# Kernel optimization log

Hardware: AMD Instinct MI355X
Metric: run time of the kernel (lower is better)

The kernel has to match this reference:

```python
import jax, jax.numpy as jnp
import numpy as np
import math

N0, E, D_IN, H, NC, UH = 4096, 65536, 128, 256, 10, 64
K1 = math.ceil(0.8 * N0)   # 3277 nodes kept by pool1
K2 = math.ceil(0.2 * K1)   # 656 nodes kept by pool2

PARAM_SHAPES = dict(
    gcn1_w=(D_IN, H), gcn1_b=(H,), pool1_w=(H,), gcn2_w=(H, H), gcn2_b=(H,), pool2_w=(H,),
    inr_w=(H, H), inr_b=(H,), ini_w=(H, H), ini_b=(H,),
    enc1_w=(1, UH), enc1_b=(UH,), enc2_w=(UH, UH), enc2_b=(UH,),
    p1_w=(UH, UH), p1_b=(UH,), p2_w=(UH, UH // 2), p2_b=(UH // 2,),
    p3_w=(UH // 2, K2 * K2), p3_b=(K2 * K2,),
    rt_w=(H, H), rt_b=(H,), it_w=(H, H), it_b=(H,),
    msg_wr=(H, H), msg_wi=(H, H),
    mc1_w=(H, H // 2), mc1_b=(H // 2,), mc2_w=(H // 2, NC), mc2_b=(NC,),
    pc1_w=(H, H // 2), pc1_b=(H // 2,), pc2_w=(H // 2, NC), pc2_b=(NC,),
)

def gcn_conv(x, src, dst, emask, W, b):
    # GCNConv: self-loops + symmetric normalization; emask zeroes edges dropped by pooling
    n = x.shape[0]
    h = x @ W
    deg = jnp.zeros((n,), h.dtype).at[dst].add(emask) + 1.0
    dis = jax.lax.rsqrt(deg)
    coef = dis[src] * dis[dst] * emask
    out = jnp.zeros_like(h).at[dst].add(coef[:, None] * h[src])
    out = out + (dis * dis)[:, None] * h   # self-loop contribution
    return out + b

def topk_pool(x, src, dst, emask, w, k):
    # PyG TopKPooling: score = x@w/||w||, keep top-k, x <- x[perm]*tanh(score[perm])
    n = x.shape[0]
    score = (x @ w) / jnp.linalg.norm(w)
    _, perm = jax.lax.top_k(score, k)
    x_new = x[perm] * jnp.tanh(score[perm])[:, None]
    mapping = jnp.full((n,), -1, jnp.int32).at[perm].set(jnp.arange(k, dtype=jnp.int32))
    ns, nd = mapping[src], mapping[dst]
    nm = emask * (ns >= 0) * (nd >= 0)
    return x_new, jnp.maximum(ns, 0), jnp.maximum(nd, 0), nm

def herm_sqrt(C):
    C = (C + C.conj().T) * 0.5
    w, V = jnp.linalg.eigh(C)
    w = jnp.maximum(w, 0.0)
    return (V * jnp.sqrt(w + 1e-8)) @ V.conj().T

def forward(x, edge_index, P):
    src, dst = edge_index[0], edge_index[1]
    em = jnp.ones((src.shape[0],), jnp.float32)
    h = jax.nn.relu(gcn_conv(x, src, dst, em, P['gcn1_w'], P['gcn1_b']))
    h, src, dst, em = topk_pool(h, src, dst, em, P['pool1_w'], K1)
    h = jax.nn.relu(gcn_conv(h, src, dst, em, P['gcn2_w'], P['gcn2_b']))
    h, src, dst, em = topk_pool(h, src, dst, em, P['pool2_w'], K2)
    xr = h @ P['inr_w'] + P['inr_b']
    xi = h @ P['ini_w'] + P['ini_b']
    # --- LocalQuantumLayer (eval mode: dropout is identity) ---
    # ImprovedUnitaryDilationNetwork on the pooled graph (N = K2)
    xg = jnp.ones((K2, 1), jnp.float32)
    xg = jax.nn.relu(gcn_conv(xg, src, dst, em, P['enc1_w'], P['enc1_b']))
    xg = gcn_conv(xg, src, dst, em, P['enc2_w'], P['enc2_b'])
    emb = xg.mean(0)                                     # global_mean_pool, single graph
    t = jax.nn.relu(emb @ P['p1_w'] + P['p1_b'])
    t = jax.nn.relu(t @ P['p2_w'] + P['p2_b'])
    pm = jnp.tanh(t @ P['p3_w'] + P['p3_b']).reshape(K2, K2)
    A = 0.05 * ((pm - pm.T) * 0.5 + 1j * (pm + pm.T) * 0.5)  # antihermitian, scaled
    U = jax.scipy.linalg.expm(A)
    I = jnp.eye(K2, dtype=U.dtype)
    S1 = jax.lax.stop_gradient(herm_sqrt(I - U.conj().T @ U))
    S2 = jax.lax.stop_gradient(herm_sqrt(I - U @ U.conj().T))
    U_dil = jnp.concatenate([jnp.concatenate([U, S1], 1),
                             jnp.concatenate([S2, -U.conj().T], 1)], 0)
    xrt = jax.nn.relu(xr @ P['rt_w'] + P['rt_b'])
    xit = jax.nn.relu(xi @ P['it_w'] + P['it_b'])
    xc = xrt + 1j * xit
    # unitary_dim = 2*K2 > K2 nodes -> single batch, U_sub = U_dil[:K2,:K2]
    evolved = U_dil[:K2, :K2] @ xc
    Wm = P['msg_wr'] + 1j * P['msg_wi']
    msg = evolved[src] @ Wm                              # message(x_j) = x_j @ W (complex)
    agg = jnp.zeros_like(xc).at[dst].add(msg * em[:, None])  # aggr='add'
    outc = agg + (xr + 1j * xi)                          # identity residual (dims equal)
    mag = jnp.abs(outc)
    ph = jnp.arctan2(outc.imag, outc.real)
    gm, gp = mag.mean(0), ph.mean(0)                     # global_mean_pool, single graph
    lm = jax.nn.relu(gm @ P['mc1_w'] + P['mc1_b']) @ P['mc2_w'] + P['mc2_b']
    lp = jax.nn.relu(gp @ P['pc1_w'] + P['pc1_b']) @ P['pc2_w'] + P['pc2_b']
    return lm + lp

def setup_inputs() -> dict:
    key = jax.random.key(0)
    ks = iter(jax.random.split(key, 64))
    inp = {}
    inp['x'] = jax.random.normal(next(ks), (N0, D_IN), jnp.float32)
    inp['edge_index'] = jax.random.randint(next(ks), (2, E), 0, N0)
    for name, shp in PARAM_SHAPES.items():
        inp[name] = jax.random.normal(next(ks), shp, jnp.float32) * 0.05
    return inp

def reference(x, edge_index, gcn1_w, gcn1_b, pool1_w, gcn2_w, gcn2_b, pool2_w, inr_w, inr_b, ini_w, ini_b, enc1_w, enc1_b, enc2_w, enc2_b, p1_w, p1_b, p2_w, p2_b, p3_w, p3_b, rt_w, rt_b, it_w, it_b, msg_wr, msg_wi, mc1_w, mc1_b, mc2_w, mc2_b, pc1_w, pc1_b, pc2_w, pc2_b):
    P = dict(locals())
    x_ = P.pop('x'); ei = P.pop('edge_index')
    return forward(x_, ei, P)
```

## Files before the change

### kernel.cpp

```cpp
#include <hip/hip_runtime.h>
#include <cstddef>
#include <utility>

constexpr int N0  = 4096;
constexpr int E   = 65536;
constexpr int DIN = 128;
constexpr int HD  = 256;
constexpr int NC  = 10;
constexpr int UHD = 64;
constexpr int K1  = 3277;
constexpr int K2  = 656;
constexpr int PMN = K2 * K2;

constexpr int SQ_SLOTS = 4;

constexpr int PLD = 704;
constexpr size_t PPS = (size_t)PLD * PLD;

constexpr int CSPLIT = 8;

#define F4(n) ((size_t)(n) * 4)
constexpr size_t O_H1    = 0;
constexpr size_t O_OUT1  = O_H1    + F4(N0 * HD);
constexpr size_t O_DEG1  = O_OUT1  + F4(N0 * HD);
constexpr size_t O_DIS1  = O_DEG1  + F4(N0);
constexpr size_t O_SC1   = O_DIS1  + F4(N0);
constexpr size_t O_PERM1 = O_SC1   + F4(N0);
constexpr size_t O_MAP1  = O_PERM1 + F4(N0);
constexpr size_t O_H1P   = O_MAP1  + F4(N0);
constexpr size_t O_SRC2  = O_H1P   + F4(K1 * HD);
constexpr size_t O_DST2  = O_SRC2  + F4(E);
constexpr size_t O_EM2   = O_DST2  + F4(E);
constexpr size_t O_H2    = O_EM2   + F4(E);
constexpr size_t O_OUT2  = O_H2    + F4(K1 * HD);
constexpr size_t O_DEG2  = O_OUT2  + F4(K1 * HD);
constexpr size_t O_DIS2  = O_DEG2  + F4(N0);
constexpr size_t O_SC2   = O_DIS2  + F4(N0);
constexpr size_t O_PERM2 = O_SC2   + F4(N0);
constexpr size_t O_MAP2  = O_PERM2 + F4(N0);
constexpr size_t O_H2P   = O_MAP2  + F4(N0);
constexpr size_t O_SRC3  = O_H2P   + F4(K2 * HD);
constexpr size_t O_DST3  = O_SRC3  + F4(E);
constexpr size_t O_EM3   = O_DST3  + F4(E);
constexpr size_t O_XR    = O_EM3   + F4(E);
constexpr size_t O_XI    = O_XR    + F4(K2 * HD);
constexpr size_t O_DEG3  = O_XI    + F4(K2 * HD);
constexpr size_t O_DIS3  = O_DEG3  + F4(1024);
constexpr size_t O_SCOEF = O_DIS3  + F4(1024);
constexpr size_t O_XG1   = O_SCOEF + F4(1024);
constexpr size_t O_XG2H  = O_XG1   + F4(K2 * UHD);
constexpr size_t O_XG2   = O_XG2H  + F4(K2 * UHD);
constexpr size_t O_EMB   = O_XG2   + F4(K2 * UHD);
constexpr size_t O_T1    = O_EMB   + F4(64);
constexpr size_t O_T2    = O_T1    + F4(64);
constexpr size_t O_NORM  = O_T2    + F4(64);
constexpr size_t O_PM    = O_NORM  + F4(64);
constexpr size_t O_BM    = O_PM    + F4(PMN);
constexpr size_t O_P0    = O_BM    + F4(PMN) * 2;
constexpr size_t O_P1    = O_P0    + F4(PMN) * 2;
constexpr size_t O_XRT   = O_P1    + F4(PMN) * 2;
constexpr size_t O_XIT   = O_XRT   + F4(K2 * HD);
constexpr size_t O_XC    = O_XIT   + F4(K2 * HD);
constexpr size_t O_EVO   = O_XC    + F4(K2 * HD) * 2;
constexpr size_t O_AGG0  = O_EVO   + F4(K2 * HD) * 2;
constexpr size_t O_WC    = O_AGG0  + F4(K2 * HD) * 2;
constexpr size_t O_AGG1  = O_WC    + F4(HD * HD) * 2;
constexpr size_t O_MAG   = O_AGG1  + F4(K2 * HD) * 2;
constexpr size_t O_PH    = O_MAG   + F4(K2 * HD);
constexpr size_t O_GM    = O_PH    + F4(K2 * HD);
constexpr size_t O_GP    = O_GM    + F4(256);
constexpr size_t O_HM    = O_GP    + F4(256);
constexpr size_t O_HP    = O_HM    + F4(256);
constexpr size_t O_LM    = O_HP    + F4(256);
constexpr size_t O_LP    = O_LM    + F4(64);
constexpr size_t WS_NEED = O_LP    + F4(64);

constexpr size_t O_SA = 0;
constexpr size_t O_ST = O_SA + PPS * 2 * 4;
static_assert(O_ST + PPS * 2 * 4 <= O_SRC3, "SA/ST must fit in dead region");

constexpr size_t O_B2 = O_XRT;
static_assert(O_B2 + F4(PMN) * 2 <= O_MAG, "B2 must fit in XRT..AGG1 region");

constexpr size_t O_CSR_OFF = O_MAG;
constexpr size_t O_CSR_CUR = O_CSR_OFF + F4(4104);
constexpr size_t O_CSR_SRC = O_CSR_CUR + F4(4104);
constexpr size_t O_CSR_CF  = O_CSR_SRC + F4(E);
static_assert(O_CSR_CF + F4(E) <= O_GM, "CSR must fit in MAG/PH region");

constexpr size_t O_PARTX  = (WS_NEED + 255) & ~(size_t)255;
constexpr size_t PART_SZ  = (size_t)CSPLIT * PMN * 8;
constexpr size_t WS_TOTAL = O_PARTX + PART_SZ;

typedef __attribute__((ext_vector_type(8))) short s8v;
typedef __attribute__((ext_vector_type(4))) float f4v;

__device__ inline unsigned short f2bf(float x) {
  unsigned u = __float_as_uint(x);
  u += 0x7FFFu + ((u >> 16) & 1u);
  return (unsigned short)(u >> 16);
}
__device__ inline float bf2f(unsigned short h) {
  return __uint_as_float(((unsigned)h) << 16);
}
__device__ inline void split4(float re, float im, unsigned short* out,
                              size_t ps, size_t o) {
  unsigned short rh = f2bf(re);
  unsigned short rl = f2bf(re - bf2f(rh));
  unsigned short ih = f2bf(im);
  unsigned short il = f2bf(im - bf2f(ih));
  out[o] = rh; out[ps + o] = rl; out[2 * ps + o] = ih; out[3 * ps + o] = il;
}


template <int ACT>
__global__ void rmm64(const float* __restrict__ A, const float* __restrict__ B,
                      const float* __restrict__ bias, float* __restrict__ C,
                      int M, int N, int K, int CS, int CO) {
  __shared__ float As[64][17];
  __shared__ float Bs[16][64];
  int t  = threadIdx.x;
  int tx = t & 15, ty = t >> 4;
  int bm = blockIdx.y * 64, bn = blockIdx.x * 64;
  float acc[4][4] = {};
  for (int kt = 0; kt < K; kt += 16) {
#pragma unroll
    for (int i = 0; i < 4; i++) {
      int l = t + i * 256;
      int kk = l & 15, mm = l >> 4;
      int gr = bm + mm;
      As[mm][kk] = (gr < M) ? A[(size_t)gr * K + kt + kk] : 0.f;
    }
#pragma unroll
    for (int i = 0; i < 4; i++) {
      int l = t + i * 256;
      int cc = l & 63, kk = l >> 6;
      int gc = bn + cc;
      Bs[kk][cc] = (gc < N) ? B[(size_t)(kt + kk) * N + gc] : 0.f;
    }
    __syncthreads();
#pragma unroll
    for (int kk = 0; kk < 16; kk++) {
      float a[4], b[4];
#pragma unroll
      for (int i = 0; i < 4; i++) a[i] = As[ty + 16 * i][kk];
#pragma unroll
      for (int j = 0; j < 4; j++) b[j] = Bs[kk][tx + 16 * j];
#pragma unroll
      for (int i = 0; i < 4; i++)
#pragma unroll
        for (int j = 0; j < 4; j++) acc[i][j] += a[i] * b[j];
    }
    __syncthreads();
  }
#pragma unroll
  for (int i = 0; i < 4; i++) {
    int r = bm + ty + 16 * i;
    if (r >= M) continue;
#pragma unroll
    for (int j = 0; j < 4; j++) {
      int c = bn + tx + 16 * j;
      if (c >= N) continue;
      float v = acc[i][j] + (bias ? bias[c] : 0.f);
      if (ACT == 1) v = fmaxf(v, 0.f);
      C[((size_t)r * N + c) * CS + CO] = v;
    }
  }
}

template <int ACT>
__global__ void rmm64_dual(const float* __restrict__ A0, const float* __restrict__ A1,
                           const float* __restrict__ B0, const float* __restrict__ B1,
                           const float* __restrict__ b0, const float* __restrict__ b1,
                           float* __restrict__ C0, float* __restrict__ C1,
                           int M, int N, int K, int CS) {
  const float* A = blockIdx.z ? A1 : A0;
  const float* B = blockIdx.z ? B1 : B0;
  const float* bias = blockIdx.z ? b1 : b0;
  float* C = blockIdx.z ? C1 : C0;
  __shared__ float As[64][17];
  __shared__ float Bs[16][64];
  int t  = threadIdx.x;
  int tx = t & 15, ty = t >> 4;
  int bm = blockIdx.y * 64, bn = blockIdx.x * 64;
  float acc[4][4] = {};
  for (int kt = 0; kt < K; kt += 16) {
#pragma unroll
    for (int i = 0; i < 4; i++) {
      int l = t + i * 256;
      int kk = l & 15, mm = l >> 4;
      int gr = bm + mm;
      As[mm][kk] = (gr < M) ? A[(size_t)gr * K + kt + kk] : 0.f;
    }
#pragma unroll
    for (int i = 0; i < 4; i++) {
      int l = t + i * 256;
      int cc = l & 63, kk = l >> 6;
      int gc = bn + cc;
      Bs[kk][cc] = (gc < N) ? B[(size_t)(kt + kk) * N + gc] : 0.f;
    }
    __syncthreads();
#pragma unroll
    for (int kk = 0; kk < 16; kk++) {
      float a[4], b[4];
#pragma unroll
      for (int i = 0; i < 4; i++) a[i] = As[ty + 16 * i][kk];
#pragma unroll
      for (int j = 0; j < 4; j++) b[j] = Bs[kk][tx + 16 * j];
#pragma unroll
      for (int i = 0; i < 4; i++)
#pragma unroll
        for (int j = 0; j < 4; j++) acc[i][j] += a[i] * b[j];
    }
    __syncthreads();
  }
#pragma unroll
  for (int i = 0; i < 4; i++) {
    int r = bm + ty + 16 * i;
    if (r >= M) continue;
#pragma unroll
    for (int j = 0; j < 4; j++) {
      int c = bn + tx + 16 * j;
      if (c >= N) continue;
      float v = acc[i][j] + (bias ? bias[c] : 0.f);
      if (ACT == 1) v = fmaxf(v, 0.f);
      C[((size_t)r * N + c) * CS] = v;
    }
  }
}

__global__ void split_planesT(const float2* __restrict__ in, int inM, int inN,
                              unsigned short* __restrict__ out, int padR, int ld,
                              size_t ps) {
  __shared__ float2 tile[32][33];
  int tx = threadIdx.x & 31, ty = threadIdx.x >> 5;
  int k0 = blockIdx.x * 32, n0 = blockIdx.y * 32;
  for (int i = ty; i < 32; i += 8) {
    int k = k0 + i, n = n0 + tx;
    tile[i][tx] = (k < inM && n < inN) ? in[(size_t)k * inN + n]
                                       : make_float2(0.f, 0.f);
  }
  __syncthreads();
  for (int i = ty; i < 32; i += 8) {
    int n = n0 + i, k = k0 + tx;
    if (n < padR && k < ld)
      split4(tile[tx][i].x, tile[tx][i].y, out, ps, (size_t)n * ld + k);
  }
}

__global__ void split_planesT2(const float* __restrict__ re, const float* __restrict__ im,
                               int inM, int inN, unsigned short* __restrict__ out,
                               int padR, int ld, size_t ps) {
  __shared__ float2 tile[32][33];
  int tx = threadIdx.x & 31, ty = threadIdx.x >> 5;
  int k0 = blockIdx.x * 32, n0 = blockIdx.y * 32;
  for (int i = ty; i < 32; i += 8) {
    int k = k0 + i, n = n0 + tx;
    tile[i][tx] = (k < inM && n < inN)
        ? make_float2(re[(size_t)k * inN + n], im[(size_t)k * inN + n])
        : make_float2(0.f, 0.f);
  }
  __syncthreads();
  for (int i = ty; i < 32; i += 8) {
    int n = n0 + i, k = k0 + tx;
    if (n < padR && k < ld)
      split4(tile[tx][i].x, tile[tx][i].y, out, ps, (size_t)n * ld + k);
  }
}

__global__ __launch_bounds__(256, 2) void cmm_bf16_sk(
    const unsigned short* __restrict__ SA, size_t psA, int ldA,
    const unsigned short* __restrict__ ST, size_t psT, int ldT,
    float2* __restrict__ Part, int M, int N, int Kp, int chunk,
    const int* __restrict__ gate, int slot) {
  if (gate && slot >= *gate - 1) return;
  int k0 = blockIdx.x * chunk;
  int kend = min(Kp, k0 + chunk);
  int t = threadIdx.x;
  int wave = t >> 6, lane = t & 63;
  int quad = lane >> 4, mn = lane & 15;
  int rowA = blockIdx.z * 64 + wave * 16 + mn;
  int bn = blockIdx.y * 64;
  const unsigned short* a0 = SA + (size_t)rowA * ldA;
  f4v accR[4], accI[4];
#pragma unroll
  for (int i = 0; i < 4; i++) {
    accR[i] = (f4v){0.f, 0.f, 0.f, 0.f};
    accI[i] = (f4v){0.f, 0.f, 0.f, 0.f};
  }
  s8v cA[4], cB[4][4], nA[4], nB[4][4];
  {
    int ka = k0 + quad * 8;
#pragma unroll
    for (int p = 0; p < 4; p++) cA[p] = *(const s8v*)(a0 + p * psA + ka);
#pragma unroll
    for (int tl = 0; tl < 4; tl++) {
      const unsigned short* b0 = ST + (size_t)(bn + tl * 16 + mn) * ldT + ka;
#pragma unroll
      for (int p = 0; p < 4; p++) cB[tl][p] = *(const s8v*)(b0 + p * psT);
    }
  }
  for (int kt = k0; kt < kend; kt += 32) {
    int kn = kt + 32;
    if (kn < kend) {
      int ka = kn + quad * 8;
#pragma unroll
      for (int p = 0; p < 4; p++) nA[p] = *(const s8v*)(a0 + p * psA + ka);
#pragma unroll
      for (int tl = 0; tl < 4; tl++) {
        const unsigned short* b0 = ST + (size_t)(bn + tl * 16 + mn) * ldT + ka;
#pragma unroll
        for (int p = 0; p < 4; p++) nB[tl][p] = *(const s8v*)(b0 + p * psT);
      }
    }
    s8v nih, nil_;
#pragma unroll
    for (int q = 0; q < 8; q++) {
      nih[q]  = (short)(cA[2][q] ^ (short)0x8000);
      nil_[q] = (short)(cA[3][q] ^ (short)0x8000);
    }
#pragma unroll
    for (int tl = 0; tl < 4; tl++) {
      f4v r = accR[tl];
      r = __builtin_amdgcn_mfma_f32_16x16x32_bf16(cA[0], cB[tl][0], r, 0, 0, 0);
      r = __builtin_amdgcn_mfma_f32_16x16x32_bf16(cA[1], cB[tl][0], r, 0, 0, 0);
      r = __builtin_amdgcn_mfma_f32_16x16x32_bf16(cA[0], cB[tl][1], r, 0, 0, 0);
      r = __builtin_amdgcn_mfma_f32_16x16x32_bf16(nih, cB[tl][2], r, 0, 0, 0);
      r = __builtin_amdgcn_mfma_f32_16x16x32_bf16(nil_, cB[tl][2], r, 0, 0, 0);
      r = __builtin_amdgcn_mfma_f32_16x16x32_bf16(nih, cB[tl][3], r, 0, 0, 0);
      accR[tl] = r;
      f4v im = accI[tl];
      im = __builtin_amdgcn_mfma_f32_16x16x32_bf16(cA[0], cB[tl][2], im, 0, 0, 0);
      im = __builtin_amdgcn_mfma_f32_16x16x32_bf16(cA[1], cB[tl][2], im, 0, 0, 0);
      im = __builtin_amdgcn_mfma_f32_16x16x32_bf16(cA[0], cB[tl][3], im, 0, 0, 0);
      im = __builtin_amdgcn_mfma_f32_16x16x32_bf16(cA[2], cB[tl][0], im, 0, 0, 0);
      im = __builtin_amdgcn_mfma_f32_16x16x32_bf16(cA[3], cB[tl][0], im, 0, 0, 0);
      im = __builtin_amdgcn_mfma_f32_16x16x32_bf16(cA[2], cB[tl][1], im, 0, 0, 0);
      accI[tl] = im;
    }
    if (kn < kend) {
#pragma unroll
      for (int p = 0; p < 4; p++) cA[p] = nA[p];
#pragma unroll
      for (int tl = 0; tl < 4; tl++)
#pragma unroll
        for (int p = 0; p < 4; p++) cB[tl][p] = nB[tl][p];
    }
  }
  float2* P = Part + (size_t)blockIdx.x * M * N;
#pragma unroll
  for (int tl = 0; tl < 4; tl++) {
    int col = bn + tl * 16 + mn;
    if (col >= N) continue;
#pragma unroll
    for (int r = 0; r < 4; r++) {
      int row = blockIdx.z * 64 + wave * 16 + quad * 4 + r;
      if (row >= M) continue;
      P[(size_t)row * N + col] = make_float2(accR[tl][r], accI[tl][r]);
    }
  }
}

__global__ void creduce(const float2* __restrict__ Part, float2* __restrict__ C,
                        int MN, int N, int S, float e0,
                        const float2* __restrict__ E1, float e1,
                        const float2* __restrict__ E2, float e2) {
  int idx = blockIdx.x * 256 + threadIdx.x;
  if (idx >= MN) return;
  float sr = 0.f, si = 0.f;
  for (int z = 0; z < S; z++) {
    float2 p = Part[(size_t)z * MN + idx];
    sr += p.x;
    si += p.y;
  }
  if (e0 != 0.f) {
    int r = idx / N;
    if (idx - r * N == r) sr += e0;
  }
  if (E1) { float2 b = E1[idx]; sr += e1 * b.x; si += e1 * b.y; }
  if (E2) { float2 b = E2[idx]; sr += e2 * b.x; si += e2 * b.y; }
  C[idx] = make_float2(sr, si);
}

template <int WC_, int WSA, int WST>
__global__ void creduce_tiled(const float2* __restrict__ Part, int S, int M, int N,
                              int RP, int CP, float2* __restrict__ C,
                              unsigned short* __restrict__ SAp, size_t psA,
                              unsigned short* __restrict__ STp, size_t psT,
                              float e0, const float2* __restrict__ E1, float e1,
                              const float2* __restrict__ E2, float e2,
                              const int* __restrict__ gate, int slot) {
  if (gate && slot >= *gate - 1) return;
  __shared__ float vr[32][33], vi[32][33];
  int tx = threadIdx.x & 31, ty = threadIdx.x >> 5;
  int r0 = blockIdx.y * 32, c0 = blockIdx.x * 32;
  size_t MN = (size_t)M * N;
  for (int i = ty; i < 32; i += 8) {
    int r = r0 + i, c = c0 + tx;
    float sr = 0.f, si = 0.f;
    if (r < M && c < N) {
      size_t o = (size_t)r * N + c;
      for (int z = 0; z < S; z++) {
        float2 p = Part[z * MN + o];
        sr += p.x;
        si += p.y;
      }
      if (e0 != 0.f && r == c) sr += e0;
      if (E1) { float2 b = E1[o]; sr += e1 * b.x; si += e1 * b.y; }
      if (E2) { float2 b = E2[o]; sr += e2 * b.x; si += e2 * b.y; }
      if (WC_) C[o] = make_float2(sr, si);
    }
    if (WSA) split4(sr, si, SAp, psA, (size_t)r * CP + c);
    if (WST) { vr[i][tx] = sr; vi[i][tx] = si; }
  }
  if (WST) {
    __syncthreads();
    for (int i = ty; i < 32; i += 8) {
      int c = c0 + i, r = r0 + tx;
      split4(vr[tx][i], vi[tx][i], STp, psT, (size_t)c * RP + r);
    }
  }
}

__global__ void build_B_split(const float* __restrict__ pm, int n,
                              const float* __restrict__ scale_p,
                              float2* __restrict__ BM,
                              unsigned short* __restrict__ SAp,
                              unsigned short* __restrict__ STp, size_t ps,
                              int RP, int CP) {
  __shared__ float vr[32][33], vi[32][33];
  float scale = scale_p[0];
  int tx = threadIdx.x & 31, ty = threadIdx.x >> 5;
  int r0 = blockIdx.y * 32, c0 = blockIdx.x * 32;
  for (int i = ty; i < 32; i += 8) {
    int r = r0 + i, c = c0 + tx;
    float sr = 0.f, si = 0.f;
    if (r < n && c < n) {
      float pij = pm[(size_t)r * n + c];
      float pji = pm[(size_t)c * n + r];
      sr = scale * (pij - pji);
      si = scale * (pij + pji);
      BM[(size_t)r * n + c] = make_float2(sr, si);
    }
    split4(sr, si, SAp, ps, (size_t)r * CP + c);
    vr[i][tx] = sr;
    vi[i][tx] = si;
  }
  __syncthreads();
  for (int i = ty; i < 32; i += 8) {
    int c = c0 + i, r = r0 + tx;
    split4(vr[tx][i], vi[tx][i], STp, ps, (size_t)c * RP + r);
  }
}

__global__ void anorm_rows(const float* __restrict__ pm, int n,
                           int* __restrict__ anrm) {
  int i = blockIdx.x;
  __shared__ float red[256];
  float s = 0.f;
  for (int j = threadIdx.x; j < n; j += 256) {
    float pij = pm[(size_t)i * n + j];
    float pji = pm[(size_t)j * n + i];
    float a = pij - pji, b = pij + pji;
    s += sqrtf(a * a + b * b);
  }
  red[threadIdx.x] = s;
  __syncthreads();
  for (int off = 128; off > 0; off >>= 1) {
    if (threadIdx.x < off) red[threadIdx.x] += red[threadIdx.x + off];
    __syncthreads();
  }
  if (threadIdx.x == 0) atomicMax(anrm, __float_as_int(red[0] * 0.025f));
}

__global__ void finalize_s(const int* __restrict__ anrm, int* __restrict__ sdev,
                           float* __restrict__ scale) {
  float a = __int_as_float(*anrm);
  int s = (int)ceilf(log2f(fmaxf(a, 1e-20f) / 1.4f));
  s = min(max(s, 1), SQ_SLOTS + 1);
  *sdev = s;
  *scale = 0.025f * exp2f(-(float)s);
}

__global__ void combo3_planes(const float2* __restrict__ Bp, const float2* __restrict__ B2p,
                              unsigned short* __restrict__ planes, size_t ps,
                              int M, int N, int padR, int ld,
                              float e0, float e1, float e2) {
  int idx = blockIdx.x * 256 + threadIdx.x;
  if (idx >= padR * ld) return;
  int r = idx / ld, c = idx - r * ld;
  float sr = 0.f, si = 0.f;
  if (r < M && c < N) {
    size_t o = (size_t)r * N + c;
    float2 b = Bp[o], b2 = B2p[o];
    sr = e1 * b.x + e2 * b2.x;
    si = e1 * b.y + e2 * b2.y;
    if (r == c) sr += e0;
  }
  split4(sr, si, planes, ps, idx);
}

__global__ void hist_edges(const int* __restrict__ dst, const float* __restrict__ em,
                           int* __restrict__ cnt) {
  int e = blockIdx.x * 256 + threadIdx.x;
  if (e >= E) return;
  float m = em ? em[e] : 1.0f;
  if (m != 0.f) atomicAdd(&cnt[dst[e]], 1);
}

__global__ __launch_bounds__(1024) void scan_offsets(const int* __restrict__ cnt, int n,
                                                     int* __restrict__ off,
                                                     int* __restrict__ cur,
                                                     float* __restrict__ dis) {
  __shared__ int sums[1024];
  int t = threadIdx.x;
  int base = t * 4;
  int v[4];
  int s = 0;
#pragma unroll
  for (int j = 0; j < 4; j++) {
    int i = base + j;
    int ci = (i < n) ? cnt[i] : 0;
    if (i < n) dis[i] = 1.0f / sqrtf((float)ci + 1.0f);
    v[j] = s;
    s += ci;
  }
  sums[t] = s;
  __syncthreads();
  for (int d = 1; d < 1024; d <<= 1) {
    int x = (t >= d) ? sums[t - d] : 0;
    __syncthreads();
    sums[t] += x;
    __syncthreads();
  }
  int pre = (t > 0) ? sums[t - 1] : 0;
#pragma unroll
  for (int j = 0; j < 4; j++) {
    int i = base + j;
    if (i < n) { int o = pre + v[j]; off[i] = o; cur[i] = o; }
  }
  if (t == 1023) off[n] = sums[1023];
}

__global__ void fill_edges(const int* __restrict__ src, const int* __restrict__ dst,
                           const float* __restrict__ em, const float* __restrict__ dis,
                           int* __restrict__ cur, int* __restrict__ esrc,
                           float* __restrict__ ecoef) {
  int e = blockIdx.x * 256 + threadIdx.x;
  if (e >= E) return;
  float m = em ? em[e] : 1.0f;
  if (m == 0.f) return;
  int s = src[e], d = dst[e];
  int pos = atomicAdd(&cur[d], 1);
  esrc[pos] = s;
  ecoef[pos] = dis[s] * dis[d];
}

template <int ACT>
__global__ void gcn_gather(const int* __restrict__ off, const int* __restrict__ esrc,
                           const float* __restrict__ ecoef, const float* __restrict__ Hm,
                           const float* __restrict__ dis, const float* __restrict__ bias,
                           float* __restrict__ out, int F) {
  int i = blockIdx.x;
  int e0 = off[i], e1 = off[i + 1];
  float d2 = dis[i] * dis[i];
  for (int f = threadIdx.x; f < F; f += blockDim.x) {
    float acc = d2 * Hm[(size_t)i * F + f] + bias[f];
    for (int e = e0; e < e1; e++)
      acc += ecoef[e] * Hm[(size_t)esrc[e] * F + f];
    if (ACT == 1) acc = fmaxf(acc, 0.f);
    out[(size_t)i * F + f] = acc;
  }
}

__global__ void enc1_fused(const int* __restrict__ off, const float* __restrict__ ecoef,
                           const float* __restrict__ dis, const float* __restrict__ w,
                           const float* __restrict__ b, float* __restrict__ xg1) {
  int i = blockIdx.x;
  int lane = threadIdx.x;
  float s = 0.f;
  for (int e = off[i] + lane; e < off[i + 1]; e += 64) s += ecoef[e];
#pragma unroll
  for (int d = 32; d > 0; d >>= 1) s += __shfl_xor(s, d, 64);
  float sc = s + dis[i] * dis[i];
  xg1[(size_t)i * UHD + lane] = fmaxf(sc * w[lane] + b[lane], 0.f);
}

__global__ void agg_gather_split(const int* __restrict__ off, const int* __restrict__ esrc,
                                 const float2* __restrict__ evo,
                                 unsigned short* __restrict__ planes, size_t ps,
                                 int F, int M) {
  int i = blockIdx.x;
  if (i >= M) {
    for (int f = threadIdx.x; f < F; f += blockDim.x)
      split4(0.f, 0.f, planes, ps, (size_t)i * F + f);
    return;
  }
  int e0 = off[i], e1 = off[i + 1];
  for (int f = threadIdx.x; f < F; f += blockDim.x) {
    float sr = 0.f, si = 0.f;
    for (int e = e0; e < e1; e++) {
      float2 v = evo[(size_t)esrc[e] * F + f];
      sr += v.x;
      si += v.y;
    }
    split4(sr, si, planes, ps, (size_t)i * F + f);
  }
}

__global__ void rowdot_wn(const float* __restrict__ X, const float* __restrict__ w,
                          float* __restrict__ out, int F, int n,
                          float* __restrict__ normout) {
  int i = blockIdx.x;
  __shared__ float red[256];
  float s = 0.f;
  if (i == n) {
    for (int k = threadIdx.x; k < F; k += 256) s += w[k] * w[k];
  } else {
    for (int f = threadIdx.x; f < F; f += 256) s += X[(size_t)i * F + f] * w[f];
  }
  red[threadIdx.x] = s;
  __syncthreads();
  for (int off = 128; off > 0; off >>= 1) {
    if (threadIdx.x < off) red[threadIdx.x] += red[threadIdx.x + off];
    __syncthreads();
  }
  if (threadIdx.x == 0) {
    if (i == n) normout[0] = sqrtf(red[0]);
    else out[i] = red[0];
  }
}

__global__ __launch_bounds__(1024) void bitonic_topk(const float* __restrict__ score,
                                                     int n, int* __restrict__ perm, int k,
                                                     int* __restrict__ map,
                                                     int* __restrict__ cntz, int ncnt) {
  __shared__ unsigned long long keys[4096];
  int t = threadIdx.x;
  for (int i = t; i < 4096; i += 1024) {
    unsigned long long kk = 0ull;
    if (i < n) {
      float f = score[i];
      unsigned u = __float_as_uint(f);
      u = (f >= 0.0f) ? (u | 0x80000000u) : ~u;
      kk = ((unsigned long long)u << 32) | (unsigned)(~(unsigned)i);
    }
    keys[i] = kk;
  }
  __syncthreads();
  for (int size = 2; size <= 4096; size <<= 1) {
    for (int stride = size >> 1; stride > 0; stride >>= 1) {
      for (int i = t; i < 2048; i += 1024) {
        int pos = ((i & ~(stride - 1)) << 1) | (i & (stride - 1));
        int partner = pos + stride;
        bool desc = (pos & size) == 0;
        unsigned long long a = keys[pos], b = keys[partner];
        if ((a < b) == desc) { keys[pos] = b; keys[partner] = a; }
      }
      __syncthreads();
    }
  }
  for (int i = t; i < 4096; i += 1024) {
    int idx = (int)(~(unsigned)(keys[i] & 0xFFFFFFFFull));
    if (idx >= 0) map[idx] = (i < k) ? i : -1;
    if (i < k) perm[i] = idx;
  }
  for (int i = t; i < ncnt; i += 1024) cntz[i] = 0;
}

__global__ void pool_gather(const float* __restrict__ X, const int* __restrict__ perm,
                            const float* __restrict__ dot, const float* __restrict__ normbuf,
                            float* __restrict__ Xn, int F) {
  int i = blockIdx.x;
  int p = perm[i];
  float sc = tanhf(dot[p] / normbuf[0]);
  for (int f = threadIdx.x; f < F; f += blockDim.x)
    Xn[(size_t)i * F + f] = X[(size_t)p * F + f] * sc;
}

__global__ void remap_hist(const int* __restrict__ srcIn, const int* __restrict__ dstIn,
                           const float* __restrict__ emIn, const int* __restrict__ map,
                           int* __restrict__ srcOut, int* __restrict__ dstOut,
                           float* __restrict__ emOut, int* __restrict__ cnt) {
  int e = blockIdx.x * 256 + threadIdx.x;
  if (e >= E) return;
  int ns = map[srcIn[e]], nd = map[dstIn[e]];
  float m = emIn ? emIn[e] : 1.0f;
  if (ns < 0 || nd < 0) m = 0.f;
  srcOut[e] = ns < 0 ? 0 : ns;
  dstOut[e] = nd < 0 ? 0 : nd;
  emOut[e] = m;
  if (m != 0.f) atomicAdd(&cnt[nd], 1);
}

__global__ void col_mean(const float* __restrict__ X, float* __restrict__ out,
                         int rows, int cols) {
  int c = blockIdx.x;
  __shared__ float red[256];
  float s = 0.f;
  for (int r = threadIdx.x; r < rows; r += 256) s += X[(size_t)r * cols + c];
  red[threadIdx.x] = s;
  __syncthreads();
  for (int off = 128; off > 0; off >>= 1) {
    if (threadIdx.x < off) red[threadIdx.x] += red[threadIdx.x + off];
    __syncthreads();
  }
  if (threadIdx.x == 0) out[c] = red[0] / (float)rows;
}

__global__ void magph_mean(const float2* __restrict__ agg, const float* __restrict__ xr,
                           const float* __restrict__ xi, float* __restrict__ gm,
                           float* __restrict__ gp, int rows, int cols) {
  int c = blockIdx.x;
  __shared__ float rm[256], rp[256];
  float sm = 0.f, sp = 0.f;
  for (int r = threadIdx.x; r < rows; r += 256) {
    size_t o = (size_t)r * cols + c;
    float2 a = agg[o];
    float re = a.x + xr[o];
    float im = a.y + xi[o];
    sm += sqrtf(re * re + im * im);
    sp += atan2f(im, re);
  }
  rm[threadIdx.x] = sm;
  rp[threadIdx.x] = sp;
  __syncthreads();
  for (int off = 128; off > 0; off >>= 1) {
    if (threadIdx.x < off) {
      rm[threadIdx.x] += rm[threadIdx.x + off];
      rp[threadIdx.x] += rp[threadIdx.x + off];
    }
    __syncthreads();
  }
  if (threadIdx.x == 0) {
    gm[c] = rm[0] / (float)rows;
    gp[c] = rp[0] / (float)rows;
  }
}

template <int ACT>
__global__ void vecmat(const float* __restrict__ v, const float* __restrict__ W,
                       const float* __restrict__ b, float* __restrict__ out,
                       int Kdim, int Ndim) {
  __shared__ float vs[256];
  for (int k = threadIdx.x; k < Kdim; k += blockDim.x) vs[k] = v[k];
  __syncthreads();
  for (int j = threadIdx.x; j < Ndim; j += blockDim.x) {
    float acc = b ? b[j] : 0.f;
    for (int k = 0; k < Kdim; k++) acc += vs[k] * W[(size_t)k * Ndim + j];
    out[j] = (ACT == 1) ? fmaxf(acc, 0.f) : acc;
  }
}

__global__ void vecmat_tanh_wide(const float* __restrict__ v, const float* __restrict__ W,
                                 const float* __restrict__ b, float* __restrict__ out,
                                 int Kdim, int Ndim, int* __restrict__ anrm_init) {
  __shared__ float vs[64];
  if (threadIdx.x < Kdim) vs[threadIdx.x] = v[threadIdx.x];
  if (blockIdx.x == 0 && threadIdx.x == 0) *anrm_init = 0;
  __syncthreads();
  int j = blockIdx.x * 256 + threadIdx.x;
  if (j >= Ndim) return;
  float acc = b[j];
  for (int k = 0; k < Kdim; k++) acc += vs[k] * W[(size_t)k * Ndim + j];
  out[j] = tanhf(acc);
}

__global__ __launch_bounds__(256) void heads_fused(
    const float* __restrict__ GM, const float* __restrict__ GP,
    const float* __restrict__ mc1_w, const float* __restrict__ mc1_b,
    const float* __restrict__ mc2_w, const float* __restrict__ mc2_b,
    const float* __restrict__ pc1_w, const float* __restrict__ pc1_b,
    const float* __restrict__ pc2_w, const float* __restrict__ pc2_b,
    float* __restrict__ out) {
  __shared__ float g[256], h[128], acc[NC];
  int t = threadIdx.x;
  if (t < NC) acc[t] = 0.f;
  for (int pass = 0; pass < 2; pass++) {
    const float* gv = pass ? GP : GM;
    const float* w1 = pass ? pc1_w : mc1_w;
    const float* b1 = pass ? pc1_b : mc1_b;
    const float* w2 = pass ? pc2_w : mc2_w;
    const float* b2 = pass ? pc2_b : mc2_b;
    g[t] = gv[t];
    __syncthreads();
    if (t < 128) {
      float s = b1[t];
      for (int k = 0; k < 256; k++) s += g[k] * w1[(size_t)k * 128 + t];
      h[t] = fmaxf(s, 0.f);
    }
    __syncthreads();
    if (t < NC) {
      float s = b2[t];
      for (int k = 0; k < 128; k++) s += h[k] * w2[(size_t)k * NC + t];
      acc[t] += s;
    }
    __syncthreads();
  }
  if (t < NC) out[t] = acc[t];
}

static inline int sk_chunk32(int K, int S) { return (((K + S - 1) / S) + 31) & ~31; }

extern "C" void kernel_launch(void* const* d_in, const int* in_sizes, int n_in,
                              void* d_out, int out_size, void* d_ws, size_t ws_size,
                              hipStream_t stream) {
  if (ws_size < WS_TOTAL) return;

  const float* x       = (const float*)d_in[0];
  const int*   ei      = (const int*)d_in[1];
  const float* gcn1_w  = (const float*)d_in[2];
  const float* gcn1_b  = (const float*)d_in[3];
  const float* pool1_w = (const float*)d_in[4];
  const float* gcn2_w  = (const float*)d_in[5];
  const float* gcn2_b  = (const float*)d_in[6];
  const float* pool2_w = (const float*)d_in[7];
  const float* inr_w   = (const float*)d_in[8];
  const float* inr_b   = (const float*)d_in[9];
  const float* ini_w   = (const float*)d_in[10];
  const float* ini_b   = (const float*)d_in[11];
  const float* enc1_w  = (const float*)d_in[12];
  const float* enc1_b  = (const float*)d_in[13];
  const float* enc2_w  = (const float*)d_in[14];
  const float* enc2_b  = (const float*)d_in[15];
  const float* p1_w    = (const float*)d_in[16];
  const float* p1_b    = (const float*)d_in[17];
  const float* p2_w    = (const float*)d_in[18];
  const float* p2_b    = (const float*)d_in[19];
  const float* p3_w    = (const float*)d_in[20];
  const float* p3_b    = (const float*)d_in[21];
  const float* rt_w    = (const float*)d_in[22];
  const float* rt_b    = (const float*)d_in[23];
  const float* it_w    = (const float*)d_in[24];
  const float* it_b    = (const float*)d_in[25];
  const float* msg_wr  = (const float*)d_in[26];
  const float* msg_wi  = (const float*)d_in[27];
  const float* mc1_w   = (const float*)d_in[28];
  const float* mc1_b   = (const float*)d_in[29];
  const float* mc2_w   = (const float*)d_in[30];
  const float* mc2_b   = (const float*)d_in[31];
  const float* pc1_w   = (const float*)d_in[32];
  const float* pc1_b   = (const float*)d_in[33];
  const float* pc2_w   = (const float*)d_in[34];
  const float* pc2_b   = (const float*)d_in[35];

  char* ws = (char*)d_ws;
  float*  H1    = (float*)(ws + O_H1);
  float*  OUT1  = (float*)(ws + O_OUT1);
  int*    CNT1  = (int*)(ws + O_DEG1);
  float*  DIS1  = (float*)(ws + O_DIS1);
  float*  SC1   = (float*)(ws + O_SC1);
  int*    PERM1 = (int*)(ws + O_PERM1);
  int*    MAP1  = (int*)(ws + O_MAP1);
  float*  H1P   = (float*)(ws + O_H1P);
  int*    SRC2  = (int*)(ws + O_SRC2);
  int*    DST2  = (int*)(ws + O_DST2);
  float*  EM2   = (float*)(ws + O_EM2);
  float*  H2    = (float*)(ws + O_H2);
  float*  OUT2  = (float*)(ws + O_OUT2);
  int*    CNT2  = (int*)(ws + O_DEG2);
  float*  DIS2  = (float*)(ws + O_DIS2);
  float*  SC2   = (float*)(ws + O_SC2);
  int*    PERM2 = (int*)(ws + O_PERM2);
  int*    MAP2  = (int*)(ws + O_MAP2);
  float*  H2P   = (float*)(ws + O_H2P);
  int*    SRC3  = (int*)(ws + O_SRC3);
  int*    DST3  = (int*)(ws + O_DST3);
  float*  EM3   = (float*)(ws + O_EM3);
  float*  XRb   = (float*)(ws + O_XR);
  float*  XIb   = (float*)(ws + O_XI);
  int*    CNT3  = (int*)(ws + O_DEG3);
  float*  DIS3  = (float*)(ws + O_DIS3);
  float*  XG1   = (float*)(ws + O_XG1);
  float*  XG2H  = (float*)(ws + O_XG2H);
  float*  XG2   = (float*)(ws + O_XG2);
  float*  EMB   = (float*)(ws + O_EMB);
  float*  T1    = (float*)(ws + O_T1);
  float*  T2    = (float*)(ws + O_T2);
  float*  NORM  = (float*)(ws + O_NORM);
  int*    ANRM  = (int*)(NORM + 2);
  int*    SDEV  = (int*)(NORM + 3);
  float*  SCALE = NORM + 4;
  float*  PMV   = (float*)(ws + O_PM);
  float2* BM    = (float2*)(ws + O_BM);
  float2* XC    = (float2*)(ws + O_XC);
  float2* EVO   = (float2*)(ws + O_EVO);
  float2* AGG1  = (float2*)(ws + O_AGG1);
  float*  GM    = (float*)(ws + O_GM);
  float*  GP    = (float*)(ws + O_GP);
  unsigned short* SA = (unsigned short*)(ws + O_SA);
  unsigned short* ST = (unsigned short*)(ws + O_ST);
  float2* PART  = (float2*)(ws + O_PARTX);
  float2* B2v   = (float2*)(ws + O_B2);
  int*    COFF  = (int*)(ws + O_CSR_OFF);
  int*    CCUR  = (int*)(ws + O_CSR_CUR);
  int*    CSRC  = (int*)(ws + O_CSR_SRC);
  float*  CCOEF = (float*)(ws + O_CSR_CF);

  const int* SRC1 = ei;
  const int* DST1 = ei + E;
  const int eg = E / 256;

  rmm64<0><<<dim3(HD / 64, N0 / 64), 256, 0, stream>>>(x, gcn1_w, nullptr, H1, N0, HD, DIN, 1, 0);
  hipMemsetAsync(CNT1, 0, F4(N0), stream);
  hist_edges<<<eg, 256, 0, stream>>>(DST1, nullptr, CNT1);
  scan_offsets<<<1, 1024, 0, stream>>>(CNT1, N0, COFF, CCUR, DIS1);
  fill_edges<<<eg, 256, 0, stream>>>(SRC1, DST1, nullptr, DIS1, CCUR, CSRC, CCOEF);
  gcn_gather<1><<<N0, 256, 0, stream>>>(COFF, CSRC, CCOEF, H1, DIS1, gcn1_b, OUT1, HD);

  rowdot_wn<<<N0 + 1, 256, 0, stream>>>(OUT1, pool1_w, SC1, HD, N0, NORM);
  bitonic_topk<<<1, 1024, 0, stream>>>(SC1, N0, PERM1, K1, MAP1, CNT2, K1);
  pool_gather<<<K1, 256, 0, stream>>>(OUT1, PERM1, SC1, NORM, H1P, HD);
  remap_hist<<<eg, 256, 0, stream>>>(SRC1, DST1, nullptr, MAP1, SRC2, DST2, EM2, CNT2);

  rmm64<0><<<dim3(HD / 64, (K1 + 63) / 64), 256, 0, stream>>>(H1P, gcn2_w, nullptr, H2, K1, HD, HD, 1, 0);
  scan_offsets<<<1, 1024, 0, stream>>>(CNT2, K1, COFF, CCUR, DIS2);
  fill_edges<<<eg, 256, 0, stream>>>(SRC2, DST2, EM2, DIS2, CCUR, CSRC, CCOEF);
  gcn_gather<1><<<K1, 256, 0, stream>>>(COFF, CSRC, CCOEF, H2, DIS2, gcn2_b, OUT2, HD);

  rowdot_wn<<<K1 + 1, 256, 0, stream>>>(OUT2, pool2_w, SC2, HD, K1, NORM + 1);
  bitonic_topk<<<1, 1024, 0, stream>>>(SC2, K1, PERM2, K2, MAP2, CNT3, K2);
  pool_gather<<<K2, 256, 0, stream>>>(OUT2, PERM2, SC2, NORM + 1, H2P, HD);
  remap_hist<<<eg, 256, 0, stream>>>(SRC2, DST2, EM2, MAP2, SRC3, DST3, EM3, CNT3);

  rmm64_dual<0><<<dim3(HD / 64, (K2 + 63) / 64, 2), 256, 0, stream>>>(
      H2P, H2P, inr_w, ini_w, inr_b, ini_b, XRb, XIb, K2, HD, HD, 1);

  scan_offsets<<<1, 1024, 0, stream>>>(CNT3, K2, COFF, CCUR, DIS3);
  fill_edges<<<eg, 256, 0, stream>>>(SRC3, DST3, EM3, DIS3, CCUR, CSRC, CCOEF);

  enc1_fused<<<K2, 64, 0, stream>>>(COFF, CCOEF, DIS3, enc1_w, enc1_b, XG1);
  rmm64<0><<<dim3(UHD / 64, (K2 + 63) / 64), 256, 0, stream>>>(XG1, enc2_w, nullptr, XG2H, K2, UHD, UHD, 1, 0);
  gcn_gather<0><<<K2, 64, 0, stream>>>(COFF, CSRC, CCOEF, XG2H, DIS3, enc2_b, XG2, UHD);
  col_mean<<<UHD, 256, 0, stream>>>(XG2, EMB, K2, UHD);

  vecmat<1><<<1, 256, 0, stream>>>(EMB, p1_w, p1_b, T1, UHD, UHD);
  vecmat<1><<<1, 256, 0, stream>>>(T1, p2_w, p2_b, T2, UHD, UHD / 2);
  vecmat_tanh_wide<<<(PMN + 255) / 256, 256, 0, stream>>>(T2, p3_w, p3_b, PMV, UHD / 2, PMN, ANRM);
  anorm_rows<<<K2, 256, 0, stream>>>(PMV, K2, ANRM);
  finalize_s<<<1, 1, 0, stream>>>(ANRM, SDEV, SCALE);

  const int sgrid = (PLD * PLD + 255) / 256;
  const dim3 tg22(PLD / 32, PLD / 32);
  const int chF = sk_chunk32(PLD, CSPLIT);
  const dim3 gBig(CSPLIT, 11, 11);
  const float c3 = 1.f / 6.f, c4 = 1.f / 24.f, c5 = 1.f / 120.f;
  const float c6 = 1.f / 720.f, c7 = 1.f / 5040.f, c8 = 1.f / 40320.f;
  const float c9 = 1.f / 362880.f, c10 = 1.f / 3628800.f, c11 = 1.f / 39916800.f;

  build_B_split<<<tg22, 256, 0, stream>>>(PMV, K2, SCALE, BM, SA, ST, PPS, PLD, PLD);
  cmm_bf16_sk<<<gBig, 256, 0, stream>>>(SA, PPS, PLD, ST, PPS, PLD, PART, K2, K2, PLD, chF, nullptr, 0);
  creduce_tiled<1, 1, 0><<<tg22, 256, 0, stream>>>(PART, CSPLIT, K2, K2, PLD, PLD,
      B2v, SA, PPS, nullptr, 0, 0.f, nullptr, 0.f, nullptr, 0.f, nullptr, 0);
  cmm_bf16_sk<<<gBig, 256, 0, stream>>>(SA, PPS, PLD, ST, PPS, PLD, PART, K2, K2, PLD, chF, nullptr, 0);
  creduce_tiled<0, 0, 1><<<tg22, 256, 0, stream>>>(PART, CSPLIT, K2, K2, PLD, PLD,
      nullptr, nullptr, 0, ST, PPS, 0.f, nullptr, 0.f, nullptr, 0.f, nullptr, 0);
  combo3_planes<<<sgrid, 256, 0, stream>>>(BM, B2v, SA, PPS, K2, K2, PLD, PLD, c9, c10, c11);
  cmm_bf16_sk<<<gBig, 256, 0, stream>>>(SA, PPS, PLD, ST, PPS, PLD, PART, K2, K2, PLD, chF, nullptr, 0);
  creduce_tiled<0, 1, 0><<<tg22, 256, 0, stream>>>(PART, CSPLIT, K2, K2, PLD, PLD,
      nullptr, SA, PPS, nullptr, 0, c6, BM, c7, B2v, c8, nullptr, 0);
  cmm_bf16_sk<<<gBig, 256, 0, stream>>>(SA, PPS, PLD, ST, PPS, PLD, PART, K2, K2, PLD, chF, nullptr, 0);
  creduce_tiled<0, 1, 0><<<tg22, 256, 0, stream>>>(PART, CSPLIT, K2, K2, PLD, PLD,
      nullptr, SA, PPS, nullptr, 0, c3, BM, c4, B2v, c5, nullptr, 0);
  cmm_bf16_sk<<<gBig, 256, 0, stream>>>(SA, PPS, PLD, ST, PPS, PLD, PART, K2, K2, PLD, chF, nullptr, 0);
  creduce_tiled<0, 1, 1><<<tg22, 256, 0, stream>>>(PART, CSPLIT, K2, K2, PLD, PLD,
      nullptr, SA, PPS, ST, PPS, 1.f, BM, 1.f, B2v, 0.5f, nullptr, 0);
  for (int t = 0; t < SQ_SLOTS; ++t) {
    cmm_bf16_sk<<<gBig, 256, 0, stream>>>(SA, PPS, PLD, ST, PPS, PLD, PART, K2, K2, PLD, chF, SDEV, t);
    creduce_tiled<0, 1, 1><<<tg22, 256, 0, stream>>>(PART, CSPLIT, K2, K2, PLD, PLD,
        nullptr, SA, PPS, ST, PPS, 0.f, nullptr, 0.f, nullptr, 0.f, SDEV, t);
  }

  rmm64_dual<1><<<dim3(HD / 64, (K2 + 63) / 64, 2), 256, 0, stream>>>(
      XRb, XIb, rt_w, it_w, rt_b, it_b, (float*)XC, (float*)XC + 1, K2, HD, HD, 2);
  {
    const int mn = K2 * HD;
    const int rg = (mn + 255) / 256;
    const dim3 gSkin(CSPLIT, HD / 64, 11);
    const size_t psX = (size_t)HD * PLD;
    split_planesT<<<dim3((PLD + 31) / 32, (HD + 31) / 32), 256, 0, stream>>>(
        XC, K2, HD, ST, HD, PLD, psX);
    cmm_bf16_sk<<<gSkin, 256, 0, stream>>>(SA, PPS, PLD, ST, psX, PLD, PART, K2, HD, PLD, chF, nullptr, 0);
    creduce_tiled<0, 0, 1><<<dim3(HD / 32, PLD / 32), 256, 0, stream>>>(
        PART, CSPLIT, K2, HD, PLD, HD, nullptr, nullptr, 0, ST, psX,
        0.f, nullptr, 0.f, nullptr, 0.f, nullptr, 0);
    cmm_bf16_sk<<<gSkin, 256, 0, stream>>>(SA, PPS, PLD, ST, psX, PLD, PART, K2, HD, PLD, chF, nullptr, 0);
    creduce<<<rg, 256, 0, stream>>>(PART, EVO, mn, HD, CSPLIT, 0.f, nullptr, 0.f, nullptr, 0.f);
    const size_t psG = (size_t)PLD * HD;
    agg_gather_split<<<PLD, 256, 0, stream>>>(COFF, CSRC, EVO, SA, psG, HD, K2);
    split_planesT2<<<dim3((HD + 31) / 32, (HD + 31) / 32), 256, 0, stream>>>(
        msg_wr, msg_wi, HD, HD, ST, HD, HD, (size_t)HD * HD);
    cmm_bf16_sk<<<gSkin, 256, 0, stream>>>(SA, psG, HD, ST, (size_t)HD * HD, HD, PART,
                                           K2, HD, HD, sk_chunk32(HD, CSPLIT), nullptr, 0);
    creduce<<<rg, 256, 0, stream>>>(PART, AGG1, mn, HD, CSPLIT, 0.f, nullptr, 0.f, nullptr, 0.f);
  }
  magph_mean<<<HD, 256, 0, stream>>>(AGG1, XRb, XIb, GM, GP, K2, HD);

  heads_fused<<<1, 256, 0, stream>>>(GM, GP, mc1_w, mc1_b, mc2_w, mc2_b,
                                     pc1_w, pc1_b, pc2_w, pc2_b, (float*)d_out);
}
```

Before: 876.9 us.

## Pick Taylor degree for matrix exponential from norm; fuse final reduce into mean

The scaled matrix norm is used to choose a lower-degree Taylor polynomial for the matrix exponential. Device-side gates skip the first one or two Horner matmul+reduce stages when the norm is small, and the combo kernel selects coefficients to match. Separately, the split-K partial sums of the final message matmul are reduced inside the magnitude/phase mean kernel, which removes a reduce launch and an intermediate buffer. Accuracy now depends on the degree thresholds, and the column-wise mean kernel makes strided passes over all partial slices.

```diff
diff --git a/kernel.cpp b/kernel.cpp
--- a/kernel.cpp
+++ b/kernel.cpp
@@ -272,8 +272,10 @@
     const unsigned short* __restrict__ SA, size_t psA, int ldA,
     const unsigned short* __restrict__ ST, size_t psT, int ldT,
     float2* __restrict__ Part, int M, int N, int Kp, int chunk,
-    const int* __restrict__ gate, int slot) {
+    const int* __restrict__ gate, int slot,
+    const int* __restrict__ dgate, int dslot) {
   if (gate && slot >= *gate - 1) return;
+  if (dgate && *dgate > dslot) return;
   int k0 = blockIdx.x * chunk;
   int kend = min(Kp, k0 + chunk);
   int t = threadIdx.x;
@@ -389,8 +391,10 @@
                               unsigned short* __restrict__ STp, size_t psT,
                               float e0, const float2* __restrict__ E1, float e1,
                               const float2* __restrict__ E2, float e2,
-                              const int* __restrict__ gate, int slot) {
+                              const int* __restrict__ gate, int slot,
+                              const int* __restrict__ dgate, int dslot) {
   if (gate && slot >= *gate - 1) return;
+  if (dgate && *dgate > dslot) return;
   __shared__ float vr[32][33], vi[32][33];
   int tx = threadIdx.x & 31, ty = threadIdx.x >> 5;
   int r0 = blockIdx.y * 32, c0 = blockIdx.x * 32;
@@ -474,18 +478,25 @@
 }
 
 __global__ void finalize_s(const int* __restrict__ anrm, int* __restrict__ sdev,
-                           float* __restrict__ scale) {
+                           float* __restrict__ scale, int* __restrict__ degf) {
   float a = __int_as_float(*anrm);
   int s = (int)ceilf(log2f(fmaxf(a, 1e-20f) / 1.4f));
   s = min(max(s, 1), SQ_SLOTS + 1);
   *sdev = s;
   *scale = 0.025f * exp2f(-(float)s);
+  float bn = a * exp2f(-(float)s);
+  *degf = (bn > 0.43f) ? 0 : (bn > 0.11f ? 1 : 2);
 }
 
 __global__ void combo3_planes(const float2* __restrict__ Bp, const float2* __restrict__ B2p,
                               unsigned short* __restrict__ planes, size_t ps,
                               int M, int N, int padR, int ld,
-                              float e0, float e1, float e2) {
+                              const int* __restrict__ degf) {
+  const float E0[3] = {1.f / 362880.f, 1.f / 720.f, 1.f / 6.f};
+  const float E1c[3] = {1.f / 3628800.f, 1.f / 5040.f, 1.f / 24.f};
+  const float E2c[3] = {1.f / 39916800.f, 1.f / 40320.f, 1.f / 120.f};
+  int f = *degf;
+  float e0 = E0[f], e1 = E1c[f], e2 = E2c[f];
   int idx = blockIdx.x * 256 + threadIdx.x;
   if (idx >= padR * ld) return;
   int r = idx / ld, c = idx - r * ld;
@@ -708,17 +719,23 @@
   if (threadIdx.x == 0) out[c] = red[0] / (float)rows;
 }
 
-__global__ void magph_mean(const float2* __restrict__ agg, const float* __restrict__ xr,
-                           const float* __restrict__ xi, float* __restrict__ gm,
-                           float* __restrict__ gp, int rows, int cols) {
+__global__ void magph_mean_part(const float2* __restrict__ Part, int S,
+                                const float* __restrict__ xr,
+                                const float* __restrict__ xi,
+                                float* __restrict__ gm, float* __restrict__ gp,
+                                int rows, int cols) {
   int c = blockIdx.x;
   __shared__ float rm[256], rp[256];
+  size_t MN = (size_t)rows * cols;
   float sm = 0.f, sp = 0.f;
   for (int r = threadIdx.x; r < rows; r += 256) {
     size_t o = (size_t)r * cols + c;
-    float2 a = agg[o];
-    float re = a.x + xr[o];
-    float im = a.y + xi[o];
+    float re = xr[o], im = xi[o];
+    for (int z = 0; z < S; z++) {
+      float2 p = Part[z * MN + o];
+      re += p.x;
+      im += p.y;
+    }
     sm += sqrtf(re * re + im * im);
     sp += atan2f(im, re);
   }
@@ -881,11 +898,11 @@
   int*    ANRM  = (int*)(NORM + 2);
   int*    SDEV  = (int*)(NORM + 3);
   float*  SCALE = NORM + 4;
+  int*    DEGF  = (int*)(NORM + 5);
   float*  PMV   = (float*)(ws + O_PM);
   float2* BM    = (float2*)(ws + O_BM);
   float2* XC    = (float2*)(ws + O_XC);
   float2* EVO   = (float2*)(ws + O_EVO);
-  float2* AGG1  = (float2*)(ws + O_AGG1);
   float*  GM    = (float*)(ws + O_GM);
   float*  GP    = (float*)(ws + O_GP);
   unsigned short* SA = (unsigned short*)(ws + O_SA);
@@ -938,7 +955,7 @@
   vecmat<1><<<1, 256, 0, stream>>>(T1, p2_w, p2_b, T2, UHD, UHD / 2);
   vecmat_tanh_wide<<<(PMN + 255) / 256, 256, 0, stream>>>(T2, p3_w, p3_b, PMV, UHD / 2, PMN, ANRM);
   anorm_rows<<<K2, 256, 0, stream>>>(PMV, K2, ANRM);
-  finalize_s<<<1, 1, 0, stream>>>(ANRM, SDEV, SCALE);
+  finalize_s<<<1, 1, 0, stream>>>(ANRM, SDEV, SCALE, DEGF);
 
   const int sgrid = (PLD * PLD + 255) / 256;
   const dim3 tg22(PLD / 32, PLD / 32);
@@ -946,29 +963,34 @@
   const dim3 gBig(CSPLIT, 11, 11);
   const float c3 = 1.f / 6.f, c4 = 1.f / 24.f, c5 = 1.f / 120.f;
   const float c6 = 1.f / 720.f, c7 = 1.f / 5040.f, c8 = 1.f / 40320.f;
-  const float c9 = 1.f / 362880.f, c10 = 1.f / 3628800.f, c11 = 1.f / 39916800.f;
 
   build_B_split<<<tg22, 256, 0, stream>>>(PMV, K2, SCALE, BM, SA, ST, PPS, PLD, PLD);
-  cmm_bf16_sk<<<gBig, 256, 0, stream>>>(SA, PPS, PLD, ST, PPS, PLD, PART, K2, K2, PLD, chF, nullptr, 0);
+  cmm_bf16_sk<<<gBig, 256, 0, stream>>>(SA, PPS, PLD, ST, PPS, PLD, PART, K2, K2, PLD, chF,
+                                        nullptr, 0, nullptr, 0);
   creduce_tiled<1, 1, 0><<<tg22, 256, 0, stream>>>(PART, CSPLIT, K2, K2, PLD, PLD,
-      B2v, SA, PPS, nullptr, 0, 0.f, nullptr, 0.f, nullptr, 0.f, nullptr, 0);
-  cmm_bf16_sk<<<gBig, 256, 0, stream>>>(SA, PPS, PLD, ST, PPS, PLD, PART, K2, K2, PLD, chF, nullptr, 0);
+      B2v, SA, PPS, nullptr, 0, 0.f, nullptr, 0.f, nullptr, 0.f, nullptr, 0, nullptr, 0);
+  cmm_bf16_sk<<<gBig, 256, 0, stream>>>(SA, PPS, PLD, ST, PPS, PLD, PART, K2, K2, PLD, chF,
+                                        nullptr, 0, nullptr, 0);
   creduce_tiled<0, 0, 1><<<tg22, 256, 0, stream>>>(PART, CSPLIT, K2, K2, PLD, PLD,
-      nullptr, nullptr, 0, ST, PPS, 0.f, nullptr, 0.f, nullptr, 0.f, nullptr, 0);
-  combo3_planes<<<sgrid, 256, 0, stream>>>(BM, B2v, SA, PPS, K2, K2, PLD, PLD, c9, c10, c11);
-  cmm_bf16_sk<<<gBig, 256, 0, stream>>>(SA, PPS, PLD, ST, PPS, PLD, PART, K2, K2, PLD, chF, nullptr, 0);
+      nullptr, nullptr, 0, ST, PPS, 0.f, nullptr, 0.f, nullptr, 0.f, nullptr, 0, nullptr, 0);
+  combo3_planes<<<sgrid, 256, 0, stream>>>(BM, B2v, SA, PPS, K2, K2, PLD, PLD, DEGF);
+  cmm_bf16_sk<<<gBig, 256, 0, stream>>>(SA, PPS, PLD, ST, PPS, PLD, PART, K2, K2, PLD, chF,
+                                        nullptr, 0, DEGF, 0);
   creduce_tiled<0, 1, 0><<<tg22, 256, 0, stream>>>(PART, CSPLIT, K2, K2, PLD, PLD,
-      nullptr, SA, PPS, nullptr, 0, c6, BM, c7, B2v, c8, nullptr, 0);
-  cmm_bf16_sk<<<gBig, 256, 0, stream>>>(SA, PPS, PLD, ST, PPS, PLD, PART, K2, K2, PLD, chF, nullptr, 0);
+      nullptr, SA, PPS, nullptr, 0, c6, BM, c7, B2v, c8, nullptr, 0, DEGF, 0);
+  cmm_bf16_sk<<<gBig, 256, 0, stream>>>(SA, PPS, PLD, ST, PPS, PLD, PART, K2, K2, PLD, chF,
+                                        nullptr, 0, DEGF, 1);
   creduce_tiled<0, 1, 0><<<tg22, 256, 0, stream>>>(PART, CSPLIT, K2, K2, PLD, PLD,
-      nullptr, SA, PPS, nullptr, 0, c3, BM, c4, B2v, c5, nullptr, 0);
-  cmm_bf16_sk<<<gBig, 256, 0, stream>>>(SA, PPS, PLD, ST, PPS, PLD, PART, K2, K2, PLD, chF, nullptr, 0);
+      nullptr, SA, PPS, nullptr, 0, c3, BM, c4, B2v, c5, nullptr, 0, DEGF, 1);
+  cmm_bf16_sk<<<gBig, 256, 0, stream>>>(SA, PPS, PLD, ST, PPS, PLD, PART, K2, K2, PLD, chF,
+                                        nullptr, 0, nullptr, 0);
   creduce_tiled<0, 1, 1><<<tg22, 256, 0, stream>>>(PART, CSPLIT, K2, K2, PLD, PLD,
-      nullptr, SA, PPS, ST, PPS, 1.f, BM, 1.f, B2v, 0.5f, nullptr, 0);
+      nullptr, SA, PPS, ST, PPS, 1.f, BM, 1.f, B2v, 0.5f, nullptr, 0, nullptr, 0);
   for (int t = 0; t < SQ_SLOTS; ++t) {
-    cmm_bf16_sk<<<gBig, 256, 0, stream>>>(SA, PPS, PLD, ST, PPS, PLD, PART, K2, K2, PLD, chF, SDEV, t);
+    cmm_bf16_sk<<<gBig, 256, 0, stream>>>(SA, PPS, PLD, ST, PPS, PLD, PART, K2, K2, PLD, chF,
+                                          SDEV, t, nullptr, 0);
     creduce_tiled<0, 1, 1><<<tg22, 256, 0, stream>>>(PART, CSPLIT, K2, K2, PLD, PLD,
-        nullptr, SA, PPS, ST, PPS, 0.f, nullptr, 0.f, nullptr, 0.f, SDEV, t);
+        nullptr, SA, PPS, ST, PPS, 0.f, nullptr, 0.f, nullptr, 0.f, SDEV, t, nullptr, 0);
   }
 
   rmm64_dual<1><<<dim3(HD / 64, (K2 + 63) / 64, 2), 256, 0, stream>>>(
@@ -980,21 +1002,23 @@
     const size_t psX = (size_t)HD * PLD;
     split_planesT<<<dim3((PLD + 31) / 32, (HD + 31) / 32), 256, 0, stream>>>(
         XC, K2, HD, ST, HD, PLD, psX);
-    cmm_bf16_sk<<<gSkin, 256, 0, stream>>>(SA, PPS, PLD, ST, psX, PLD, PART, K2, HD, PLD, chF, nullptr, 0);
+    cmm_bf16_sk<<<gSkin, 256, 0, stream>>>(SA, PPS, PLD, ST, psX, PLD, PART, K2, HD, PLD, chF,
+                                           nullptr, 0, nullptr, 0);
     creduce_tiled<0, 0, 1><<<dim3(HD / 32, PLD / 32), 256, 0, stream>>>(
         PART, CSPLIT, K2, HD, PLD, HD, nullptr, nullptr, 0, ST, psX,
-        0.f, nullptr, 0.f, nullptr, 0.f, nullptr, 0);
-    cmm_bf16_sk<<<gSkin, 256, 0, stream>>>(SA, PPS, PLD, ST, psX, PLD, PART, K2, HD, PLD, chF, nullptr, 0);
+        0.f, nullptr, 0.f, nullptr, 0.f, nullptr, 0, nullptr, 0);
+    cmm_bf16_sk<<<gSkin, 256, 0, stream>>>(SA, PPS, PLD, ST, psX, PLD, PART, K2, HD, PLD, chF,
+                                           nullptr, 0, nullptr, 0);
     creduce<<<rg, 256, 0, stream>>>(PART, EVO, mn, HD, CSPLIT, 0.f, nullptr, 0.f, nullptr, 0.f);
     const size_t psG = (size_t)PLD * HD;
     agg_gather_split<<<PLD, 256, 0, stream>>>(COFF, CSRC, EVO, SA, psG, HD, K2);
     split_planesT2<<<dim3((HD + 31) / 32, (HD + 31) / 32), 256, 0, stream>>>(
         msg_wr, msg_wi, HD, HD, ST, HD, HD, (size_t)HD * HD);
     cmm_bf16_sk<<<gSkin, 256, 0, stream>>>(SA, psG, HD, ST, (size_t)HD * HD, HD, PART,
-                                           K2, HD, HD, sk_chunk32(HD, CSPLIT), nullptr, 0);
-    creduce<<<rg, 256, 0, stream>>>(PART, AGG1, mn, HD, CSPLIT, 0.f, nullptr, 0.f, nullptr, 0.f);
-  }
-  magph_mean<<<HD, 256, 0, stream>>>(AGG1, XRb, XIb, GM, GP, K2, HD);
+                                           K2, HD, HD, sk_chunk32(HD, CSPLIT),
+                                           nullptr, 0, nullptr, 0);
+    magph_mean_part<<<HD, 256, 0, stream>>>(PART, CSPLIT, XRb, XIb, GM, GP, K2, HD);
+  }
 
   heads_fused<<<1, 256, 0, stream>>>(GM, GP, mc1_w, mc1_b, mc2_w, mc2_b,
                                      pc1_w, pc1_b, pc2_w, pc2_b, (float*)d_out);
```

Measured after the change: 900.4 us. 1.03x slower.
